# Kernel tuning notes

Hardware: AMD Instinct MI355X
Metric: run time of the kernel (lower is better)

Reference implementation:

```python
import jax, jax.numpy as jnp
import numpy as np
from jax import lax

B, C, T = 32, 512, 2000
G, I, H = 8, 64, 64  # groups, per-group input size, per-group hidden size


def setup_inputs() -> dict:
    key = jax.random.key(0)
    k = jax.random.split(key, 5)
    s = 1.0 / np.sqrt(H)  # torch GRU init scale
    return {
        "x": jax.random.normal(k[0], (B, C, T), dtype=jnp.float32),
        "h0": jnp.zeros((G, B, H), dtype=jnp.float32),
        "w_ih": jax.random.uniform(k[1], (G, 3 * H, I), jnp.float32, -s, s),
        "w_hh": jax.random.uniform(k[2], (G, 3 * H, H), jnp.float32, -s, s),
        "b_ih": jax.random.uniform(k[3], (G, 3 * H), jnp.float32, -s, s),
        "b_hh": jax.random.uniform(k[4], (G, 3 * H), jnp.float32, -s, s),
    }


def _grouped_gru(x, h0, w_ih, w_hh, b_ih, b_hh):
    # x: [B, C, T] -> [T, B, G, I]
    xg = x.transpose(2, 0, 1).reshape(T, B, G, I)
    # Precompute input projections for all timesteps: [T, B, G, 3H]
    x_proj = jnp.einsum("tbgi,gki->tbgk", xg, w_ih) + b_ih
    h_init = h0.transpose(1, 0, 2)  # [B, G, H]

    def step(h, xp):
        # h: [B, G, H]; xp: [B, G, 3H]
        hp = jnp.einsum("bgh,gkh->bgk", h, w_hh) + b_hh
        xr, xz, xn = jnp.split(xp, 3, axis=-1)
        hr, hz, hn = jnp.split(hp, 3, axis=-1)
        r = jax.nn.sigmoid(xr + hr)
        z = jax.nn.sigmoid(xz + hz)
        n = jnp.tanh(xn + r * hn)
        h_new = (1.0 - z) * n + z * h
        return h_new, h_new

    h_last, ys = lax.scan(step, h_init, x_proj)  # ys: [T, B, G, H]
    out = ys.reshape(T, B, G * H).transpose(1, 2, 0)  # [B, G*H, T]
    return out, h_last


def reference(x, h0, w_ih, w_hh, b_ih, b_hh):
    out, _ = _grouped_gru(x, h0, w_ih, w_hh, b_ih, b_hh)
    return out
```

## Files before the change

kernel.cpp:

```cpp
#include <hip/hip_runtime.h>
#include <cstddef>


constexpr int B_ = 32;
constexpr int C_ = 512;
constexpr int T_ = 2000;
constexpr int G_ = 8;
constexpr int I_ = 64;
constexpr int H_ = 64;
constexpr int K3_ = 3 * H_;

template <int CTRL>
__device__ __forceinline__ float dpp_xadd(float v) {
    int p = __builtin_amdgcn_update_dpp(0, __float_as_int(v), CTRL, 0xF, 0xF, true);
    return v + __int_as_float(p);
}
__device__ __forceinline__ float reduce8(float v) {
    v = dpp_xadd<0xB1>(v);
    v = dpp_xadd<0x4E>(v);
    v = dpp_xadd<0x141>(v);
    return v;
}

__device__ __forceinline__ float sigmoid_f(float x) {
    float e = __expf(-x);
    return __builtin_amdgcn_rcpf(1.0f + e);
}
__device__ __forceinline__ float tanh_f(float x) {
    float e = __expf(2.0f * x);
    return 1.0f - 2.0f * __builtin_amdgcn_rcpf(e + 1.0f);
}

__global__ __launch_bounds__(512, 1)
void gru_scan_kernel(const float* __restrict__ x,
                     const float* __restrict__ h0,
                     const float* __restrict__ w_ih,
                     const float* __restrict__ w_hh,
                     const float* __restrict__ b_ih,
                     const float* __restrict__ b_hh,
                     float* __restrict__ out)
{
    const int bid = blockIdx.x;
    const int g = bid & (G_ - 1);
    const int b = bid >> 3;
    const int tid = threadIdx.x;
    const int j = tid >> 3;
    const int sub = tid & 7;

    __shared__ float h_s[2][H_];
    __shared__ float xbuf[2][I_];

    float wir[8], wiz[8], win[8], whr[8], whz[8], whn[8];
    {
        const size_t rowbase = (size_t)g * K3_ + j;
        const float* pir = w_ih + (rowbase          ) * I_ + sub * 8;
        const float* piz = w_ih + (rowbase +     H_ ) * I_ + sub * 8;
        const float* pin = w_ih + (rowbase + 2 * H_ ) * I_ + sub * 8;
        const float* phr = w_hh + (rowbase          ) * H_ + sub * 8;
        const float* phz = w_hh + (rowbase +     H_ ) * H_ + sub * 8;
        const float* phn = w_hh + (rowbase + 2 * H_ ) * H_ + sub * 8;
        #pragma unroll
        for (int q = 0; q < 2; ++q) {
            float4 a;
            a = reinterpret_cast<const float4*>(pir)[q];
            wir[4*q+0]=a.x; wir[4*q+1]=a.y; wir[4*q+2]=a.z; wir[4*q+3]=a.w;
            a = reinterpret_cast<const float4*>(piz)[q];
            wiz[4*q+0]=a.x; wiz[4*q+1]=a.y; wiz[4*q+2]=a.z; wiz[4*q+3]=a.w;
            a = reinterpret_cast<const float4*>(pin)[q];
            win[4*q+0]=a.x; win[4*q+1]=a.y; win[4*q+2]=a.z; win[4*q+3]=a.w;
            a = reinterpret_cast<const float4*>(phr)[q];
            whr[4*q+0]=a.x; whr[4*q+1]=a.y; whr[4*q+2]=a.z; whr[4*q+3]=a.w;
            a = reinterpret_cast<const float4*>(phz)[q];
            whz[4*q+0]=a.x; whz[4*q+1]=a.y; whz[4*q+2]=a.z; whz[4*q+3]=a.w;
            a = reinterpret_cast<const float4*>(phn)[q];
            whn[4*q+0]=a.x; whn[4*q+1]=a.y; whn[4*q+2]=a.z; whn[4*q+3]=a.w;
        }
    }
    const float brc = b_ih[g * K3_ + j]            + b_hh[g * K3_ + j];
    const float bzc = b_ih[g * K3_ + H_ + j]       + b_hh[g * K3_ + H_ + j];
    const float bin = b_ih[g * K3_ + 2 * H_ + j];
    const float bhn = b_hh[g * K3_ + 2 * H_ + j];

    const float* xbase = x + ((size_t)b * C_ + (size_t)g * I_) * T_;
    float* outbase = out + ((size_t)b * (G_ * H_) + (size_t)g * H_) * T_;

    if (tid < H_) {
        h_s[0][tid] = h0[((size_t)g * B_ + b) * H_ + tid];
        xbuf[0][tid] = xbase[(size_t)tid * T_];
        xbuf[1][tid] = xbase[(size_t)tid * T_ + 1];
    }
    __syncthreads();

    float xr_s = 0.f, xz_s = 0.f, xn_s = 0.f;
    {
        const float* xp = &xbuf[0][sub * 8];
        #pragma unroll
        for (int i = 0; i < 8; ++i) {
            float xv = xp[i];
            xr_s = fmaf(wir[i], xv, xr_s);
            xz_s = fmaf(wiz[i], xv, xz_s);
            xn_s = fmaf(win[i], xv, xn_s);
        }
    }
    __syncthreads();

    for (int t = 0; t < T_; ++t) {
        const int cur = t & 1, nxt = cur ^ 1;

        float hr = 0.f, hz = 0.f, hn = 0.f;
        {
            const float* hp = &h_s[cur][sub * 8];
            #pragma unroll
            for (int i = 0; i < 8; ++i) {
                float hv = hp[i];
                hr = fmaf(whr[i], hv, hr);
                hz = fmaf(whz[i], hv, hz);
                hn = fmaf(whn[i], hv, hn);
            }
        }
        const float h_old = h_s[cur][j];

        float xr2 = 0.f, xz2 = 0.f, xn2 = 0.f;
        {
            const float* xp = &xbuf[nxt][sub * 8];
            #pragma unroll
            for (int i = 0; i < 8; ++i) {
                float xv = xp[i];
                xr2 = fmaf(wir[i], xv, xr2);
                xz2 = fmaf(wiz[i], xv, xz2);
                xn2 = fmaf(win[i], xv, xn2);
            }
        }

        float xg = 0.f;
        if (tid < I_ && t + 2 < T_) xg = xbase[(size_t)tid * T_ + (t + 2)];

        const float pre_r  = reduce8(xr_s + hr);
        const float pre_z  = reduce8(xz_s + hz);
        const float xn_sum = reduce8(xn_s);
        const float hn_sum = reduce8(hn);

        const float r = sigmoid_f(pre_r + brc);
        const float z = sigmoid_f(pre_z + bzc);
        const float n = tanh_f(xn_sum + bin + r * (hn_sum + bhn));
        const float hnew = (1.0f - z) * n + z * h_old;

        if (sub == 0) {
            h_s[nxt][j] = hnew;
            outbase[(size_t)j * T_ + t] = hnew;
        }
        if (tid < I_) xbuf[cur][tid] = xg;

        xr_s = xr2; xz_s = xz2; xn_s = xn2;
        __syncthreads();
    }
}

extern "C" void kernel_launch(void* const* d_in, const int* in_sizes, int n_in,
                              void* d_out, int out_size, void* d_ws, size_t ws_size,
                              hipStream_t stream)
{
    const float* x    = (const float*)d_in[0];
    const float* h0   = (const float*)d_in[1];
    const float* w_ih = (const float*)d_in[2];
    const float* w_hh = (const float*)d_in[3];
    const float* b_ih = (const float*)d_in[4];
    const float* b_hh = (const float*)d_in[5];
    float* out = (float*)d_out;

    dim3 grid(B_ * G_);
    dim3 block(512);
    gru_scan_kernel<<<grid, block, 0, stream>>>(x, h0, w_ih, w_hh, b_ih, b_hh, out);
}
```

Before: 914.2 us.

## Use packed fp16 dot products and halve threads per GRU block

Weights, hidden state and inputs are converted to fp16 and the matvecs use v_dot2 fp16 instructions accumulating in fp32. Each thread now covers 16 elements, so a block has 256 threads and the cross-lane reduction needs only two DPP steps. This is meant to shorten the serial per-step latency and barrier cost of the recurrence. The risk is accuracy loss from fp16 weights and hidden state compounding over 2000 recurrent steps.

```diff
diff --git a/kernel.cpp b/kernel.cpp
--- a/kernel.cpp
+++ b/kernel.cpp
@@ -1,6 +1,8 @@
 #include <hip/hip_runtime.h>
 #include <cstddef>
 
+
+typedef _Float16 h2 __attribute__((ext_vector_type(2)));
 
 constexpr int B_ = 32;
 constexpr int C_ = 512;
@@ -15,10 +17,9 @@
     int p = __builtin_amdgcn_update_dpp(0, __float_as_int(v), CTRL, 0xF, 0xF, true);
     return v + __int_as_float(p);
 }
-__device__ __forceinline__ float reduce8(float v) {
+__device__ __forceinline__ float reduce4(float v) {
     v = dpp_xadd<0xB1>(v);
     v = dpp_xadd<0x4E>(v);
-    v = dpp_xadd<0x141>(v);
     return v;
 }
 
@@ -31,7 +32,24 @@
     return 1.0f - 2.0f * __builtin_amdgcn_rcpf(e + 1.0f);
 }
 
-__global__ __launch_bounds__(512, 1)
+__device__ __forceinline__ float fdot2_(h2 a, h2 b, float c) {
+#if __has_builtin(__builtin_amdgcn_fdot2)
+    return __builtin_amdgcn_fdot2(a, b, c, false);
+#else
+    return fmaf((float)a[0], (float)b[0], fmaf((float)a[1], (float)b[1], c));
+#endif
+}
+
+__device__ __forceinline__ void ld_h2x8(const _Float16* p, h2* d) {
+    const float4* p4 = reinterpret_cast<const float4*>(p);
+    float4 a = p4[0], b = p4[1];
+    d[0] = __builtin_bit_cast(h2, a.x); d[1] = __builtin_bit_cast(h2, a.y);
+    d[2] = __builtin_bit_cast(h2, a.z); d[3] = __builtin_bit_cast(h2, a.w);
+    d[4] = __builtin_bit_cast(h2, b.x); d[5] = __builtin_bit_cast(h2, b.y);
+    d[6] = __builtin_bit_cast(h2, b.z); d[7] = __builtin_bit_cast(h2, b.w);
+}
+
+__global__ __launch_bounds__(256, 1)
 void gru_scan_kernel(const float* __restrict__ x,
                      const float* __restrict__ h0,
                      const float* __restrict__ w_ih,
@@ -44,40 +62,40 @@
     const int g = bid & (G_ - 1);
     const int b = bid >> 3;
     const int tid = threadIdx.x;
-    const int j = tid >> 3;
-    const int sub = tid & 7;
+    const int j = tid >> 2;
+    const int sub = tid & 3;
 
-    __shared__ float h_s[2][H_];
-    __shared__ float xbuf[2][I_];
+    __shared__ __align__(16) _Float16 h_h[2][H_];
+    __shared__ float h_f[2][H_];
+    __shared__ __align__(16) _Float16 xbuf[2][I_];
 
-    float wir[8], wiz[8], win[8], whr[8], whz[8], whn[8];
+    h2 Wir[8], Wiz[8], Win[8], Whr[8], Whz[8], Whn[8];
     {
-        const size_t rowbase = (size_t)g * K3_ + j;
-        const float* pir = w_ih + (rowbase          ) * I_ + sub * 8;
-        const float* piz = w_ih + (rowbase +     H_ ) * I_ + sub * 8;
-        const float* pin = w_ih + (rowbase + 2 * H_ ) * I_ + sub * 8;
-        const float* phr = w_hh + (rowbase          ) * H_ + sub * 8;
-        const float* phz = w_hh + (rowbase +     H_ ) * H_ + sub * 8;
-        const float* phn = w_hh + (rowbase + 2 * H_ ) * H_ + sub * 8;
-        #pragma unroll
-        for (int q = 0; q < 2; ++q) {
-            float4 a;
-            a = reinterpret_cast<const float4*>(pir)[q];
-            wir[4*q+0]=a.x; wir[4*q+1]=a.y; wir[4*q+2]=a.z; wir[4*q+3]=a.w;
-            a = reinterpret_cast<const float4*>(piz)[q];
-            wiz[4*q+0]=a.x; wiz[4*q+1]=a.y; wiz[4*q+2]=a.z; wiz[4*q+3]=a.w;
-            a = reinterpret_cast<const float4*>(pin)[q];
-            win[4*q+0]=a.x; win[4*q+1]=a.y; win[4*q+2]=a.z; win[4*q+3]=a.w;
-            a = reinterpret_cast<const float4*>(phr)[q];
-            whr[4*q+0]=a.x; whr[4*q+1]=a.y; whr[4*q+2]=a.z; whr[4*q+3]=a.w;
-            a = reinterpret_cast<const float4*>(phz)[q];
-            whz[4*q+0]=a.x; whz[4*q+1]=a.y; whz[4*q+2]=a.z; whz[4*q+3]=a.w;
-            a = reinterpret_cast<const float4*>(phn)[q];
-            whn[4*q+0]=a.x; whn[4*q+1]=a.y; whn[4*q+2]=a.z; whn[4*q+3]=a.w;
-        }
+        const size_t rb = (size_t)g * K3_ + j;
+        auto loadrow = [&](const float* p, h2* w) {
+            const float4* p4 = reinterpret_cast<const float4*>(p);
+            #pragma unroll
+            for (int q = 0; q < 4; ++q) {
+                float4 a = p4[q];
+                w[2*q+0] = h2{(_Float16)a.x, (_Float16)a.y};
+                w[2*q+1] = h2{(_Float16)a.z, (_Float16)a.w};
+            }
+        };
+        loadrow(w_ih + (rb           ) * I_ + sub * 16, Wir);
+        loadrow(w_ih + (rb +     H_  ) * I_ + sub * 16, Wiz);
+        loadrow(w_ih + (rb + 2 * H_  ) * I_ + sub * 16, Win);
+        loadrow(w_hh + (rb           ) * H_ + sub * 16, Whr);
+        loadrow(w_hh + (rb +     H_  ) * H_ + sub * 16, Whz);
+        loadrow(w_hh + (rb + 2 * H_  ) * H_ + sub * 16, Whn);
     }
-    const float brc = b_ih[g * K3_ + j]            + b_hh[g * K3_ + j];
-    const float bzc = b_ih[g * K3_ + H_ + j]       + b_hh[g * K3_ + H_ + j];
+    #pragma unroll
+    for (int i = 0; i < 8; ++i) {
+        asm volatile("" : "+v"(Wir[i]), "+v"(Wiz[i]), "+v"(Win[i]),
+                          "+v"(Whr[i]), "+v"(Whz[i]), "+v"(Whn[i]));
+    }
+
+    const float brc = b_ih[g * K3_ + j]           + b_hh[g * K3_ + j];
+    const float bzc = b_ih[g * K3_ + H_ + j]      + b_hh[g * K3_ + H_ + j];
     const float bin = b_ih[g * K3_ + 2 * H_ + j];
     const float bhn = b_hh[g * K3_ + 2 * H_ + j];
 
@@ -85,21 +103,22 @@
     float* outbase = out + ((size_t)b * (G_ * H_) + (size_t)g * H_) * T_;
 
     if (tid < H_) {
-        h_s[0][tid] = h0[((size_t)g * B_ + b) * H_ + tid];
-        xbuf[0][tid] = xbase[(size_t)tid * T_];
-        xbuf[1][tid] = xbase[(size_t)tid * T_ + 1];
+        float hv = h0[((size_t)g * B_ + b) * H_ + tid];
+        h_f[0][tid] = hv;
+        h_h[0][tid] = (_Float16)hv;
+        xbuf[0][tid] = (_Float16)xbase[(size_t)tid * T_];
+        xbuf[1][tid] = (_Float16)xbase[(size_t)tid * T_ + 1];
     }
     __syncthreads();
 
     float xr_s = 0.f, xz_s = 0.f, xn_s = 0.f;
     {
-        const float* xp = &xbuf[0][sub * 8];
+        h2 xv[8]; ld_h2x8(&xbuf[0][sub * 16], xv);
         #pragma unroll
         for (int i = 0; i < 8; ++i) {
-            float xv = xp[i];
-            xr_s = fmaf(wir[i], xv, xr_s);
-            xz_s = fmaf(wiz[i], xv, xz_s);
-            xn_s = fmaf(win[i], xv, xn_s);
+            xr_s = fdot2_(Wir[i], xv[i], xr_s);
+            xz_s = fdot2_(Wiz[i], xv[i], xz_s);
+            xn_s = fdot2_(Win[i], xv[i], xn_s);
         }
     }
     __syncthreads();
@@ -107,49 +126,44 @@
     for (int t = 0; t < T_; ++t) {
         const int cur = t & 1, nxt = cur ^ 1;
 
+        h2 hv[8]; ld_h2x8(&h_h[cur][sub * 16], hv);
         float hr = 0.f, hz = 0.f, hn = 0.f;
-        {
-            const float* hp = &h_s[cur][sub * 8];
-            #pragma unroll
-            for (int i = 0; i < 8; ++i) {
-                float hv = hp[i];
-                hr = fmaf(whr[i], hv, hr);
-                hz = fmaf(whz[i], hv, hz);
-                hn = fmaf(whn[i], hv, hn);
-            }
+        #pragma unroll
+        for (int i = 0; i < 8; ++i) {
+            hr = fdot2_(Whr[i], hv[i], hr);
+            hz = fdot2_(Whz[i], hv[i], hz);
+            hn = fdot2_(Whn[i], hv[i], hn);
         }
-        const float h_old = h_s[cur][j];
+        const float h_old = h_f[cur][j];
 
+        h2 xv[8]; ld_h2x8(&xbuf[nxt][sub * 16], xv);
         float xr2 = 0.f, xz2 = 0.f, xn2 = 0.f;
-        {
-            const float* xp = &xbuf[nxt][sub * 8];
-            #pragma unroll
-            for (int i = 0; i < 8; ++i) {
-                float xv = xp[i];
-                xr2 = fmaf(wir[i], xv, xr2);
-                xz2 = fmaf(wiz[i], xv, xz2);
-                xn2 = fmaf(win[i], xv, xn2);
-            }
+        #pragma unroll
+        for (int i = 0; i < 8; ++i) {
+            xr2 = fdot2_(Wir[i], xv[i], xr2);
+            xz2 = fdot2_(Wiz[i], xv[i], xz2);
+            xn2 = fdot2_(Win[i], xv[i], xn2);
         }
 
         float xg = 0.f;
         if (tid < I_ && t + 2 < T_) xg = xbase[(size_t)tid * T_ + (t + 2)];
 
-        const float pre_r  = reduce8(xr_s + hr);
-        const float pre_z  = reduce8(xz_s + hz);
-        const float xn_sum = reduce8(xn_s);
-        const float hn_sum = reduce8(hn);
+        const float pre_r  = reduce4(xr_s + hr) + brc;
+        const float pre_z  = reduce4(xz_s + hz) + bzc;
+        const float xn_sum = reduce4(xn_s) + bin;
+        const float hn_sum = reduce4(hn) + bhn;
 
-        const float r = sigmoid_f(pre_r + brc);
-        const float z = sigmoid_f(pre_z + bzc);
-        const float n = tanh_f(xn_sum + bin + r * (hn_sum + bhn));
+        const float r = sigmoid_f(pre_r);
+        const float z = sigmoid_f(pre_z);
+        const float n = tanh_f(xn_sum + r * hn_sum);
         const float hnew = (1.0f - z) * n + z * h_old;
 
         if (sub == 0) {
-            h_s[nxt][j] = hnew;
+            h_f[nxt][j] = hnew;
+            h_h[nxt][j] = (_Float16)hnew;
             outbase[(size_t)j * T_ + t] = hnew;
         }
-        if (tid < I_) xbuf[cur][tid] = xg;
+        if (tid < I_) xbuf[cur][tid] = (_Float16)xg;
 
         xr_s = xr2; xz_s = xz2; xn_s = xn2;
         __syncthreads();
@@ -169,6 +183,6 @@
     float* out = (float*)d_out;
 
     dim3 grid(B_ * G_);
-    dim3 block(512);
+    dim3 block(256);
     gru_scan_kernel<<<grid, block, 0, stream>>>(x, h0, w_ih, w_hh, b_ih, b_hh, out);
 }
```

Result: faster. 795.0 us (-13.0%).
